# Kernel optimization log

Measured on AMD Instinct MI355X. Metric: run time of the kernel, lower is better.

The kernel has to match this reference:

```python
import jax, jax.numpy as jnp
import numpy as np

N_NODES = 50000
N_EDGES = 1600000
F_IN, F_LAT, F_EMB = 128, 256, 128
N_GRAPHS = 64


def _linear_init(key, out_dim, in_dim):
    scale = 1.0 / np.sqrt(in_dim)
    return jax.random.uniform(key, (out_dim, in_dim), jnp.float32, -scale, scale)


def setup_inputs() -> dict:
    key = jax.random.key(0)
    ks = jax.random.split(key, 12)
    x = jax.random.normal(ks[0], (N_NODES, F_IN), jnp.float32)
    edge_index = jax.random.randint(ks[1], (2, N_EDGES), 0, N_NODES, jnp.int64)
    batch = jnp.sort(jax.random.randint(ks[2], (N_NODES,), 0, N_GRAPHS, jnp.int64))
    return {
        'x': x,
        'edge_index': edge_index,
        'batch': batch,
        'W1l': _linear_init(ks[3], F_LAT, F_IN),
        'b1': jnp.zeros((F_LAT,), jnp.float32),
        'W1r': _linear_init(ks[4], F_LAT, F_IN),
        'W2l': _linear_init(ks[5], F_LAT, F_LAT),
        'b2': jnp.zeros((F_LAT,), jnp.float32),
        'W2r': _linear_init(ks[6], F_LAT, F_LAT),
        'W3l': _linear_init(ks[7], F_EMB, F_LAT),
        'b3': jnp.zeros((F_EMB,), jnp.float32),
        'W3r': _linear_init(ks[8], F_EMB, F_LAT),
    }


def _sage_conv(x, src, dst, deg_inv, Wl, bl, Wr):
    # mean aggregation of neighbor features: scatter-add then divide by in-degree
    agg = jax.ops.segment_sum(x[src], dst, num_segments=N_NODES) * deg_inv
    # PyG SAGEConv: lin_l(agg) + lin_r(x); lin_l has bias, lin_r does not
    return agg @ Wl.T + bl + x @ Wr.T


def reference(x, edge_index, batch, W1l, b1, W1r, W2l, b2, W2r, W3l, b3, W3r):
    src, dst = edge_index[0], edge_index[1]
    deg = jax.ops.segment_sum(jnp.ones((N_EDGES,), jnp.float32), dst, num_segments=N_NODES)
    deg_inv = jnp.where(deg > 0, 1.0 / deg, 0.0)[:, None]  # [N,1]
    h = jax.nn.relu(_sage_conv(x, src, dst, deg_inv, W1l, b1, W1r))
    h = jax.nn.relu(_sage_conv(h, src, dst, deg_inv, W2l, b2, W2r))
    h = jax.nn.relu(_sage_conv(h, src, dst, deg_inv, W3l, b3, W3r))
    # global_add_pool: per-graph sum over nodes
    return jax.ops.segment_sum(h, batch, num_segments=N_GRAPHS)
```

## Files before the change

kernel.cpp:

```cpp
#include <hip/hip_runtime.h>
#include <hip/hip_bf16.h>

#define N_NODES 50000
#define N_EDGES 1600000
#define N_GRAPHS 64

#define NBKT 250
#define BKT_NODES 200
#define BKT_CAP 7168
#define CHUNK 4096
#define NBB 391
#define NCVX 6250
#define NCVW 256
#define ZROW N_NODES

typedef short bf16x8 __attribute__((ext_vector_type(8)));
typedef float f32x4 __attribute__((ext_vector_type(4)));
typedef float f32x2 __attribute__((ext_vector_type(2)));

__device__ __forceinline__ float bf_lo(unsigned int u) { return __uint_as_float(u << 16); }
__device__ __forceinline__ float bf_hi(unsigned int u) { return __uint_as_float(u & 0xffff0000u); }
__device__ __forceinline__ unsigned short f2bf(float f) {
    unsigned int u = __float_as_uint(f);
    u = (u + 0x7fffu + ((u >> 16) & 1u)) >> 16;
    return (unsigned short)u;
}
__device__ __forceinline__ unsigned int pack2bf(float a, float b) {
    return (unsigned int)f2bf(a) | ((unsigned int)f2bf(b) << 16);
}
__device__ __forceinline__ unsigned int pack4fp8(float a, float b, float c, float d) {
    unsigned int q = __builtin_amdgcn_cvt_pk_fp8_f32(a, b, 0, false);
    q = __builtin_amdgcn_cvt_pk_fp8_f32(c, d, q, true);
    return q;
}
__device__ __forceinline__ void load_lds16(const void* g, void* l) {
    __builtin_amdgcn_global_load_lds(
        (const __attribute__((address_space(1))) void*)g,
        (__attribute__((address_space(3))) void*)l, 16, 0, 0);
}

__global__ __launch_bounds__(256) void k_front(
    const int* __restrict__ src, const int* __restrict__ dst,
    unsigned int* __restrict__ bucketed, int* __restrict__ gcnt,
    const float* __restrict__ x, unsigned short* __restrict__ A1x,
    unsigned char* __restrict__ x8,
    const float* __restrict__ W1l, const float* __restrict__ W1r,
    const float* __restrict__ W2l, const float* __restrict__ W2r,
    const float* __restrict__ W3l, const float* __restrict__ W3r,
    unsigned short* __restrict__ Wp1, unsigned short* __restrict__ Wp2,
    unsigned short* __restrict__ Wp3) {
    const int blk = blockIdx.x;
    const int t = threadIdx.x;

    if (blk < NBB) {
        __shared__ int lcnt[256];
        __shared__ int sc[256];
        __shared__ int lscan[256];
        __shared__ int gb[256];
        __shared__ unsigned int grouped[CHUNK];

        const int base = blk * CHUNK;
        const int ccnt = min(CHUNK, N_EDGES - base);
        lcnt[t] = 0;
        __syncthreads();

        unsigned int pk[CHUNK / 256];
        int rk[CHUNK / 256];
#pragma unroll
        for (int r = 0; r < CHUNK / 256; ++r) {
            int j = r * 256 + t;
            rk[r] = -1;
            if (j < ccnt) {
                int i = base + j;
                int s = src[i];
                int d = dst[i];
                int b = d / BKT_NODES;
                int dl = d - b * BKT_NODES;
                pk[r] = (unsigned int)s | ((unsigned int)dl << 16) | ((unsigned int)b << 24);
                rk[r] = atomicAdd(&lcnt[b], 1);
            }
        }
        __syncthreads();
        sc[t] = lcnt[t];
        __syncthreads();
        for (int off = 1; off < 256; off <<= 1) {
            int v = (t >= off) ? sc[t - off] : 0;
            __syncthreads();
            sc[t] += v;
            __syncthreads();
        }
        lscan[t] = sc[t] - lcnt[t];
        if (t < NBKT && lcnt[t] > 0) gb[t] = atomicAdd(&gcnt[t], lcnt[t]);
        __syncthreads();
#pragma unroll
        for (int r = 0; r < CHUNK / 256; ++r) {
            if (rk[r] >= 0) {
                int b = pk[r] >> 24;
                grouped[lscan[b] + rk[r]] = pk[r];
            }
        }
        __syncthreads();
#pragma unroll
        for (int r = 0; r < CHUNK / 256; ++r) {
            int j = r * 256 + t;
            if (j < ccnt) {
                unsigned int v = grouped[j];
                int b = v >> 24;
                int pos = gb[b] + (j - lscan[b]);
                if (pos < BKT_CAP) bucketed[b * BKT_CAP + pos] = v;
            }
        }
    } else if (blk < NBB + NCVX) {
        int i = (blk - NBB) * 256 + t;
        int r = i >> 5;
        int f4 = (i & 31) << 2;
        float4 v = *(const float4*)&x[(size_t)r * 128 + f4];
        uint2 o;
        o.x = pack2bf(v.x, v.y);
        o.y = pack2bf(v.z, v.w);
        *(uint2*)&A1x[(size_t)r * 256 + f4] = o;
        *(unsigned int*)&x8[(size_t)r * 128 + f4] = pack4fp8(v.x, v.y, v.z, v.w);
    } else {
        int i = (blk - NBB - NCVX) * 256 + t;
        const float* srcp;
        unsigned short* dstp;
        int sf4, dstride;
        if (i < 16384) {
            int h = i >> 13;
            i &= 8191;
            srcp = h ? W1r : W1l;
            dstp = Wp1 + (h ? 128 : 0);
            sf4 = 32; dstride = 256;
        } else if (i < 49152) {
            int j = i - 16384;
            int h = j >> 14;
            i = j & 16383;
            srcp = h ? W2r : W2l;
            dstp = Wp2 + (h ? 256 : 0);
            sf4 = 64; dstride = 512;
        } else {
            int j = i - 49152;
            int h = j >> 13;
            i = j & 8191;
            srcp = h ? W3r : W3l;
            dstp = Wp3 + (h ? 128 * 256 : 0);
            sf4 = 64; dstride = 256;
        }
        int r = i / sf4;
        int f4 = (i % sf4) * 4;
        float4 v = *(const float4*)&srcp[(size_t)r * (sf4 * 4) + f4];
        uint2 o;
        o.x = pack2bf(v.x, v.y);
        o.y = pack2bf(v.z, v.w);
        *(uint2*)&dstp[(size_t)r * dstride + f4] = o;
    }
}

__global__ __launch_bounds__(512) void k_place(const unsigned int* __restrict__ bucketed,
                                               const int* __restrict__ gcnt,
                                               int* __restrict__ offs,
                                               unsigned short* __restrict__ deg,
                                               unsigned short* __restrict__ ssrc) {
    __shared__ unsigned int ent[BKT_CAP];
    __shared__ unsigned short rks[BKT_CAP];
    __shared__ int lcnt[256];
    __shared__ int sc[256];
    __shared__ int lofs[256];
    __shared__ int gs;

    const int b = blockIdx.x;
    const int t = threadIdx.x;

    if (t < 256) sc[t] = (t < NBKT) ? (gcnt[t] + 3 * BKT_NODES) : 0;
    __syncthreads();
    for (int off = 1; off < 256; off <<= 1) {
        int u = 0;
        if (t < 256 && t >= off) u = sc[t - off];
        __syncthreads();
        if (t < 256) sc[t] += u;
        __syncthreads();
    }
    if (t == 0) gs = (b == 0) ? 0 : sc[b - 1];
    if (t < 256) lcnt[t] = 0;
    __syncthreads();

    const int cnt = min(gcnt[b], BKT_CAP);
    const unsigned int* eg = bucketed + (size_t)b * BKT_CAP;
    for (int i = t; i < cnt; i += 512) {
        unsigned int v = eg[i];
        ent[i] = v;
        int dl = (v >> 16) & 0xFF;
        rks[i] = (unsigned short)atomicAdd(&lcnt[dl], 1);
    }
    __syncthreads();
    int pc = 0;
    if (t < 256) {
        pc = (lcnt[t] + 3) & ~3;
        sc[t] = pc;
    }
    __syncthreads();
    for (int off = 1; off < 256; off <<= 1) {
        int u = 0;
        if (t < 256 && t >= off) u = sc[t - off];
        __syncthreads();
        if (t < 256) sc[t] += u;
        __syncthreads();
    }
    if (t < 256) lofs[t] = sc[t] - pc;
    __syncthreads();
    const int gstart = gs;
    if (t < BKT_NODES) {
        offs[b * BKT_NODES + t] = gstart + lofs[t];
        deg[b * BKT_NODES + t] = (unsigned short)lcnt[t];
    }
    for (int i = t; i < cnt; i += 512) {
        unsigned int v = ent[i];
        int dl = (v >> 16) & 0xFF;
        ssrc[gstart + lofs[dl] + (int)rks[i]] = (unsigned short)(v & 0xFFFF);
    }
    if (t < BKT_NODES) {
        int d = lcnt[t], pd = (d + 3) & ~3;
        int base = gstart + lofs[t];
        for (int j = d; j < pd; ++j) ssrc[base + j] = (unsigned short)ZROW;
    }
}

#define DEC_ADD(dw, base)                                             \
    {                                                                 \
        f32x2 lo_ = __builtin_amdgcn_cvt_pk_f32_fp8((dw), false);     \
        f32x2 hi_ = __builtin_amdgcn_cvt_pk_f32_fp8((dw), true);      \
        a[(base) + 0] += lo_.x;                                       \
        a[(base) + 1] += lo_.y;                                       \
        a[(base) + 2] += hi_.x;                                       \
        a[(base) + 3] += hi_.y;                                       \
    }

template <int F>
__global__ __launch_bounds__(256) void k_gather8(const unsigned char* __restrict__ in,
                                                 unsigned short* __restrict__ out,
                                                 int ostride,
                                                 const int* __restrict__ offs,
                                                 const unsigned short* __restrict__ deg,
                                                 const unsigned short* __restrict__ ssrc) {
    constexpr int TPN = F / 16;
    constexpr int NPB = 256 / TPN;
    int n = blockIdx.x * NPB + threadIdx.x / TPN;
    int f16 = (threadIdx.x % TPN) * 16;
    if (n >= N_NODES) return;
    int s0 = offs[n];
    int d = deg[n];
    int pd = (d + 3) & ~3;
    float a[16];
#pragma unroll
    for (int j = 0; j < 16; ++j) a[j] = 0.f;
    const unsigned char* inf = in + f16;
    for (int i = s0; i < s0 + pd; i += 4) {
        int e0 = ssrc[i], e1 = ssrc[i + 1], e2 = ssrc[i + 2], e3 = ssrc[i + 3];
        uint4 v0 = *(const uint4*)&inf[(size_t)e0 * F];
        uint4 v1 = *(const uint4*)&inf[(size_t)e1 * F];
        uint4 v2 = *(const uint4*)&inf[(size_t)e2 * F];
        uint4 v3 = *(const uint4*)&inf[(size_t)e3 * F];
        DEC_ADD(v0.x, 0) DEC_ADD(v0.y, 4) DEC_ADD(v0.z, 8) DEC_ADD(v0.w, 12)
        DEC_ADD(v1.x, 0) DEC_ADD(v1.y, 4) DEC_ADD(v1.z, 8) DEC_ADD(v1.w, 12)
        DEC_ADD(v2.x, 0) DEC_ADD(v2.y, 4) DEC_ADD(v2.z, 8) DEC_ADD(v2.w, 12)
        DEC_ADD(v3.x, 0) DEC_ADD(v3.y, 4) DEC_ADD(v3.z, 8) DEC_ADD(v3.w, 12)
    }
    float scl = (d > 0) ? 1.f / (float)d : 0.f;
    uint4 o0, o1;
    o0.x = pack2bf(a[0] * scl, a[1] * scl);
    o0.y = pack2bf(a[2] * scl, a[3] * scl);
    o0.z = pack2bf(a[4] * scl, a[5] * scl);
    o0.w = pack2bf(a[6] * scl, a[7] * scl);
    o1.x = pack2bf(a[8] * scl, a[9] * scl);
    o1.y = pack2bf(a[10] * scl, a[11] * scl);
    o1.z = pack2bf(a[12] * scl, a[13] * scl);
    o1.w = pack2bf(a[14] * scl, a[15] * scl);
    *(uint4*)&out[(size_t)n * ostride + f16] = o0;
    *(uint4*)&out[(size_t)n * ostride + f16 + 8] = o1;
}

template <int KSTEPS, bool RELU, bool BIAS, int FP8W>
__global__ __launch_bounds__(256) void k_gemm_mfma(const unsigned short* __restrict__ A,
                                                   const unsigned short* __restrict__ W,
                                                   const float* __restrict__ bias,
                                                   unsigned short* __restrict__ C,
                                                   int ldc, int coff,
                                                   unsigned char* __restrict__ fp8out,
                                                   int M) {
    constexpr int K = KSTEPS * 64;
    __shared__ unsigned short SH[32768];

    const int tid = threadIdx.x;
    const int lane = tid & 63;
    const int w = tid >> 6;
    const int row0 = blockIdx.x * 128;
    const int colb = blockIdx.y * 128;

    const int srow_b = w * 32 + (lane >> 3);
    const int slot = lane & 7;

    f32x4 acc[4][4];
#pragma unroll
    for (int i = 0; i < 4; ++i)
#pragma unroll
        for (int j = 0; j < 4; ++j) acc[i][j] = (f32x4){0.f, 0.f, 0.f, 0.f};

    const int m0 = (w >> 1) * 64;
    const int n0 = (w & 1) * 64;

    auto STAGE = [&](int b, int ks) {
        const int kk0 = ks * 64;
#pragma unroll
        for (int it = 0; it < 4; ++it) {
            int r = srow_b + it * 8;
            int sl = (slot ^ (r & 7)) << 3;
            int ra = min(row0 + r, M - 1);
            load_lds16(A + (size_t)ra * K + kk0 + sl,
                       (char*)SH + b * 16384 + w * 4096 + it * 1024);
            load_lds16(W + (size_t)(colb + r) * K + kk0 + sl,
                       (char*)SH + 32768 + b * 16384 + w * 4096 + it * 1024);
        }
    };

    STAGE(0, 0);
    __syncthreads();
    int cur = 0;

    for (int ks = 0; ks < KSTEPS; ++ks) {
        if (ks + 1 < KSTEPS) STAGE(cur ^ 1, ks + 1);

        const char* Ab = (const char*)SH + cur * 16384;
        const char* Wb = (const char*)SH + 32768 + cur * 16384;
        bf16x8 af[4][2], bfr[4][2];
#pragma unroll
        for (int mf = 0; mf < 4; ++mf)
#pragma unroll
            for (int kk = 0; kk < 2; ++kk) {
                int r = m0 + mf * 16 + (lane & 15);
                int sl = (kk * 4 + (lane >> 4)) ^ (r & 7);
                af[mf][kk] = *(const bf16x8*)(Ab + r * 128 + sl * 16);
            }
#pragma unroll
        for (int nf = 0; nf < 4; ++nf)
#pragma unroll
            for (int kk = 0; kk < 2; ++kk) {
                int r = n0 + nf * 16 + (lane & 15);
                int sl = (kk * 4 + (lane >> 4)) ^ (r & 7);
                bfr[nf][kk] = *(const bf16x8*)(Wb + r * 128 + sl * 16);
            }
#pragma unroll
        for (int mf = 0; mf < 4; ++mf)
#pragma unroll
            for (int nf = 0; nf < 4; ++nf)
#pragma unroll
                for (int kk = 0; kk < 2; ++kk)
                    acc[mf][nf] = __builtin_amdgcn_mfma_f32_16x16x32_bf16(
                        af[mf][kk], bfr[nf][kk], acc[mf][nf], 0, 0, 0);
        __syncthreads();
        cur ^= 1;
    }

    const bool do8 = (FP8W > 0) && (colb < FP8W);

#pragma unroll
    for (int mf = 0; mf < 4; ++mf) {
#pragma unroll
        for (int nf = 0; nf < 4; ++nf) {
            int cl = n0 + nf * 16 + (lane & 15);
            int c = colb + cl;
            float bv = 0.f;
            if constexpr (BIAS) bv = bias[c];
#pragma unroll
            for (int r = 0; r < 4; ++r) {
                int ml = m0 + mf * 16 + ((lane >> 4) << 2) + r;
                int m = row0 + ml;
                if (m < M) {
                    float v = acc[mf][nf][r] + bv;
                    if constexpr (RELU) v = fmaxf(v, 0.f);
                    unsigned short bf = f2bf(v);
                    C[(size_t)m * ldc + coff + c] = bf;
                    if constexpr (FP8W > 0)
                        if (do8) SH[ml * 136 + cl] = bf;
                }
            }
        }
    }

    if constexpr (FP8W > 0) {
        if (do8) {
            __syncthreads();
#pragma unroll
            for (int q0 = 0; q0 < 1024; q0 += 256) {
                int q = q0 + tid;
                int row = q >> 3;
                int m = row0 + row;
                if (m < M) {
                    int cg = (q & 7) << 4;
                    const unsigned short* tp = SH + row * 136 + cg;
                    uint4 w0 = *(const uint4*)tp;
                    uint4 w1 = *(const uint4*)(tp + 8);
                    uint4 o;
                    o.x = pack4fp8(bf_lo(w0.x), bf_hi(w0.x), bf_lo(w0.y), bf_hi(w0.y));
                    o.y = pack4fp8(bf_lo(w0.z), bf_hi(w0.z), bf_lo(w0.w), bf_hi(w0.w));
                    o.z = pack4fp8(bf_lo(w1.x), bf_hi(w1.x), bf_lo(w1.y), bf_hi(w1.y));
                    o.w = pack4fp8(bf_lo(w1.z), bf_hi(w1.z), bf_lo(w1.w), bf_hi(w1.w));
                    *(uint4*)&fp8out[(size_t)m * FP8W + colb + cg] = o;
                }
            }
        }
    }
}

__global__ __launch_bounds__(256) void k_final8(const unsigned char* __restrict__ t3l8,
                                                const unsigned short* __restrict__ t3,
                                                const float* __restrict__ b3,
                                                const int* __restrict__ offs,
                                                const unsigned short* __restrict__ deg,
                                                const unsigned short* __restrict__ ssrc,
                                                const int* __restrict__ batch,
                                                float* __restrict__ out) {
    __shared__ float sm[16][128];
    __shared__ int bsh[16];
    const int t = threadIdx.x;
    const int sub = t >> 4;
    const int f8 = (t & 15) * 8;
    const int n = blockIdx.x * 16 + sub;

    int s0 = offs[n];
    int d = deg[n];
    int pd = (d + 3) & ~3;
    float a[8];
#pragma unroll
    for (int j = 0; j < 8; ++j) a[j] = 0.f;
    const unsigned char* inf = t3l8 + f8;
    for (int i = s0; i < s0 + pd; i += 4) {
        int e0 = ssrc[i], e1 = ssrc[i + 1], e2 = ssrc[i + 2], e3 = ssrc[i + 3];
        uint2 v0 = *(const uint2*)&inf[(size_t)e0 * 128];
        uint2 v1 = *(const uint2*)&inf[(size_t)e1 * 128];
        uint2 v2 = *(const uint2*)&inf[(size_t)e2 * 128];
        uint2 v3 = *(const uint2*)&inf[(size_t)e3 * 128];
        DEC_ADD(v0.x, 0) DEC_ADD(v0.y, 4)
        DEC_ADD(v1.x, 0) DEC_ADD(v1.y, 4)
        DEC_ADD(v2.x, 0) DEC_ADD(v2.y, 4)
        DEC_ADD(v3.x, 0) DEC_ADD(v3.y, 4)
    }
    float scl = (d > 0) ? 1.f / (float)d : 0.f;
    float4 bv0 = *(const float4*)&b3[f8];
    float4 bv1 = *(const float4*)&b3[f8 + 4];
    uint4 tr = *(const uint4*)&t3[(size_t)n * 256 + 128 + f8];
    float tv[8] = {bf_lo(tr.x), bf_hi(tr.x), bf_lo(tr.y), bf_hi(tr.y),
                   bf_lo(tr.z), bf_hi(tr.z), bf_lo(tr.w), bf_hi(tr.w)};
    float bb[8] = {bv0.x, bv0.y, bv0.z, bv0.w, bv1.x, bv1.y, bv1.z, bv1.w};
#pragma unroll
    for (int j = 0; j < 8; ++j)
        sm[sub][f8 + j] = fmaxf(a[j] * scl + bb[j] + tv[j], 0.f);
    if ((t & 15) == 0) bsh[sub] = batch[n];
    __syncthreads();

    if (t < 128) {
        float local = 0.f;
        int cur = -1;
#pragma unroll
        for (int k = 0; k < 16; ++k) {
            int b = bsh[k];
            if (b != cur) {
                if (cur >= 0) atomicAdd(&out[(size_t)cur * 128 + t], local);
                local = 0.f;
                cur = b;
            }
            local += sm[k][t];
        }
        if (cur >= 0) atomicAdd(&out[(size_t)cur * 128 + t], local);
    }
}

extern "C" void kernel_launch(void* const* d_in, const int* in_sizes, int n_in,
                              void* d_out, int out_size, void* d_ws, size_t ws_size,
                              hipStream_t stream) {
    const float* x   = (const float*)d_in[0];
    const int* ei    = (const int*)d_in[1];
    const int* batch = (const int*)d_in[2];
    const float* W1l = (const float*)d_in[3];
    const float* b1  = (const float*)d_in[4];
    const float* W1r = (const float*)d_in[5];
    const float* W2l = (const float*)d_in[6];
    const float* b2  = (const float*)d_in[7];
    const float* W2r = (const float*)d_in[8];
    const float* W3l = (const float*)d_in[9];
    const float* b3  = (const float*)d_in[10];
    const float* W3r = (const float*)d_in[11];
    const int* src = ei;
    const int* dst = ei + N_EDGES;
    float* out = (float*)d_out;

    size_t off = 0;
    auto carve = [&](size_t bytes) {
        void* p = (char*)d_ws + off;
        off += (bytes + 255) & ~(size_t)255;
        return p;
    };
    int* gcnt   = (int*)carve(256 * 4);
    int* offs   = (int*)carve((size_t)N_NODES * 4);
    unsigned short* deg  = (unsigned short*)carve((size_t)N_NODES * 2);
    unsigned short* ssrc = (unsigned short*)carve((size_t)(N_EDGES + NBKT * 3 * BKT_NODES) * 2);
    unsigned short* A1   = (unsigned short*)carve((size_t)N_NODES * 256 * 2);
    unsigned short* A2   = (unsigned short*)carve((size_t)N_NODES * 512 * 2);
    unsigned short* A3   = (unsigned short*)carve((size_t)N_NODES * 256 * 2);
    void* t3region = carve((size_t)N_NODES * 256 * 2);
    unsigned int* bucketed = (unsigned int*)t3region;
    unsigned short* t3 = (unsigned short*)t3region;
    unsigned char* x8   = (unsigned char*)carve((size_t)(N_NODES + 1) * 128);
    unsigned char* h18  = (unsigned char*)carve((size_t)(N_NODES + 1) * 256);
    unsigned char* t3l8 = (unsigned char*)carve((size_t)(N_NODES + 1) * 128);
    unsigned short* Wp1 = (unsigned short*)carve((size_t)256 * 256 * 2);
    unsigned short* Wp2 = (unsigned short*)carve((size_t)256 * 512 * 2);
    unsigned short* Wp3 = (unsigned short*)carve((size_t)256 * 256 * 2);

    hipMemsetAsync(gcnt, 0, 256 * 4, stream);
    hipMemsetAsync(d_out, 0, (size_t)out_size * 4, stream);
    hipMemsetAsync(x8 + (size_t)ZROW * 128, 0, 128, stream);
    hipMemsetAsync(h18 + (size_t)ZROW * 256, 0, 256, stream);
    hipMemsetAsync(t3l8 + (size_t)ZROW * 128, 0, 128, stream);

    k_front<<<NBB + NCVX + NCVW, 256, 0, stream>>>(src, dst, bucketed, gcnt,
                                                   x, A1 + 128, x8,
                                                   W1l, W1r, W2l, W2r, W3l, W3r,
                                                   Wp1, Wp2, Wp3);
    k_place<<<NBKT, 512, 0, stream>>>(bucketed, gcnt, offs, deg, ssrc);

    const dim3 ggrid((N_NODES + 127) / 128, 2);

    k_gather8<128><<<(N_NODES + 31) / 32, 256, 0, stream>>>(x8, A1, 256, offs, deg, ssrc);
    k_gemm_mfma<4, true, true, 256><<<ggrid, 256, 0, stream>>>(A1, Wp1, b1, A2, 512, 256, h18, N_NODES);

    k_gather8<256><<<(N_NODES + 15) / 16, 256, 0, stream>>>(h18, A2, 512, offs, deg, ssrc);
    k_gemm_mfma<8, true, true, 0><<<ggrid, 256, 0, stream>>>(A2, Wp2, b2, A3, 256, 0, nullptr, N_NODES);

    k_gemm_mfma<4, false, false, 128><<<ggrid, 256, 0, stream>>>(A3, Wp3, nullptr, t3, 256, 0, t3l8, N_NODES);
    k_final8<<<N_NODES / 16, 256, 0, stream>>>(t3l8, t3, b3, offs, deg, ssrc, batch, out);
}
```

Before: 319.8 us.

## Software-pipeline gather loops, vectorize index loads, fold zero-row memsets into front kernel

The gather kernels now prefetch the next group of four neighbor rows before accumulating the current group. They load four source indices with a single ushort4 read, which needs bucket offsets aligned to four. To keep that alignment, k_place rounds each bucket count up to a multiple of four, and the ssrc allocation grows to match. Three small memset launches for the zero padding rows are replaced by writes inside k_front. Together these aim to hide gather latency and cut launch overhead, at the cost of more live registers.

Measured after the change: 314.1 us. About the same (-1.8%).

```diff
diff --git a/kernel.cpp b/kernel.cpp
--- a/kernel.cpp
+++ b/kernel.cpp
@@ -43,7 +43,8 @@
     const int* __restrict__ src, const int* __restrict__ dst,
     unsigned int* __restrict__ bucketed, int* __restrict__ gcnt,
     const float* __restrict__ x, unsigned short* __restrict__ A1x,
-    unsigned char* __restrict__ x8,
+    unsigned char* __restrict__ x8, unsigned char* __restrict__ h18,
+    unsigned char* __restrict__ t3l8,
     const float* __restrict__ W1l, const float* __restrict__ W1r,
     const float* __restrict__ W2l, const float* __restrict__ W2r,
     const float* __restrict__ W3l, const float* __restrict__ W3r,
@@ -120,6 +121,12 @@
         o.y = pack2bf(v.z, v.w);
         *(uint2*)&A1x[(size_t)r * 256 + f4] = o;
         *(unsigned int*)&x8[(size_t)r * 128 + f4] = pack4fp8(v.x, v.y, v.z, v.w);
+        if (blk == NBB && t < 32) {
+            uint4 z = make_uint4(0, 0, 0, 0);
+            if (t < 8) *(uint4*)&x8[(size_t)ZROW * 128 + t * 16] = z;
+            else if (t < 24) *(uint4*)&h18[(size_t)ZROW * 256 + (t - 8) * 16] = z;
+            else *(uint4*)&t3l8[(size_t)ZROW * 128 + (t - 24) * 16] = z;
+        }
     } else {
         int i = (blk - NBB - NCVX) * 256 + t;
         const float* srcp;
@@ -171,7 +178,7 @@
     const int b = blockIdx.x;
     const int t = threadIdx.x;
 
-    if (t < 256) sc[t] = (t < NBKT) ? (gcnt[t] + 3 * BKT_NODES) : 0;
+    if (t < 256) sc[t] = (t < NBKT) ? (((gcnt[t] + 3) & ~3) + 3 * BKT_NODES) : 0;
     __syncthreads();
     for (int off = 1; off < 256; off <<= 1) {
         int u = 0;
@@ -234,6 +241,7 @@
         a[(base) + 2] += hi_.x;                                       \
         a[(base) + 3] += hi_.y;                                       \
     }
+#define DEC_ADD4(v) { DEC_ADD((v).x, 0) DEC_ADD((v).y, 4) DEC_ADD((v).z, 8) DEC_ADD((v).w, 12) }
 
 template <int F>
 __global__ __launch_bounds__(256) void k_gather8(const unsigned char* __restrict__ in,
@@ -254,16 +262,22 @@
 #pragma unroll
     for (int j = 0; j < 16; ++j) a[j] = 0.f;
     const unsigned char* inf = in + f16;
-    for (int i = s0; i < s0 + pd; i += 4) {
-        int e0 = ssrc[i], e1 = ssrc[i + 1], e2 = ssrc[i + 2], e3 = ssrc[i + 3];
-        uint4 v0 = *(const uint4*)&inf[(size_t)e0 * F];
-        uint4 v1 = *(const uint4*)&inf[(size_t)e1 * F];
-        uint4 v2 = *(const uint4*)&inf[(size_t)e2 * F];
-        uint4 v3 = *(const uint4*)&inf[(size_t)e3 * F];
-        DEC_ADD(v0.x, 0) DEC_ADD(v0.y, 4) DEC_ADD(v0.z, 8) DEC_ADD(v0.w, 12)
-        DEC_ADD(v1.x, 0) DEC_ADD(v1.y, 4) DEC_ADD(v1.z, 8) DEC_ADD(v1.w, 12)
-        DEC_ADD(v2.x, 0) DEC_ADD(v2.y, 4) DEC_ADD(v2.z, 8) DEC_ADD(v2.w, 12)
-        DEC_ADD(v3.x, 0) DEC_ADD(v3.y, 4) DEC_ADD(v3.z, 8) DEC_ADD(v3.w, 12)
+    if (pd > 0) {
+        ushort4 es = *(const ushort4*)&ssrc[s0];
+        uint4 c0 = *(const uint4*)&inf[(size_t)es.x * F];
+        uint4 c1 = *(const uint4*)&inf[(size_t)es.y * F];
+        uint4 c2 = *(const uint4*)&inf[(size_t)es.z * F];
+        uint4 c3 = *(const uint4*)&inf[(size_t)es.w * F];
+        for (int i = s0 + 4; i < s0 + pd; i += 4) {
+            ushort4 ns = *(const ushort4*)&ssrc[i];
+            uint4 n0 = *(const uint4*)&inf[(size_t)ns.x * F];
+            uint4 n1 = *(const uint4*)&inf[(size_t)ns.y * F];
+            uint4 n2 = *(const uint4*)&inf[(size_t)ns.z * F];
+            uint4 n3 = *(const uint4*)&inf[(size_t)ns.w * F];
+            DEC_ADD4(c0) DEC_ADD4(c1) DEC_ADD4(c2) DEC_ADD4(c3)
+            c0 = n0; c1 = n1; c2 = n2; c3 = n3;
+        }
+        DEC_ADD4(c0) DEC_ADD4(c1) DEC_ADD4(c2) DEC_ADD4(c3)
     }
     float scl = (d > 0) ? 1.f / (float)d : 0.f;
     uint4 o0, o1;
@@ -433,16 +447,28 @@
 #pragma unroll
     for (int j = 0; j < 8; ++j) a[j] = 0.f;
     const unsigned char* inf = t3l8 + f8;
-    for (int i = s0; i < s0 + pd; i += 4) {
-        int e0 = ssrc[i], e1 = ssrc[i + 1], e2 = ssrc[i + 2], e3 = ssrc[i + 3];
-        uint2 v0 = *(const uint2*)&inf[(size_t)e0 * 128];
-        uint2 v1 = *(const uint2*)&inf[(size_t)e1 * 128];
-        uint2 v2 = *(const uint2*)&inf[(size_t)e2 * 128];
-        uint2 v3 = *(const uint2*)&inf[(size_t)e3 * 128];
-        DEC_ADD(v0.x, 0) DEC_ADD(v0.y, 4)
-        DEC_ADD(v1.x, 0) DEC_ADD(v1.y, 4)
-        DEC_ADD(v2.x, 0) DEC_ADD(v2.y, 4)
-        DEC_ADD(v3.x, 0) DEC_ADD(v3.y, 4)
+    if (pd > 0) {
+        ushort4 es = *(const ushort4*)&ssrc[s0];
+        uint2 c0 = *(const uint2*)&inf[(size_t)es.x * 128];
+        uint2 c1 = *(const uint2*)&inf[(size_t)es.y * 128];
+        uint2 c2 = *(const uint2*)&inf[(size_t)es.z * 128];
+        uint2 c3 = *(const uint2*)&inf[(size_t)es.w * 128];
+        for (int i = s0 + 4; i < s0 + pd; i += 4) {
+            ushort4 ns = *(const ushort4*)&ssrc[i];
+            uint2 n0 = *(const uint2*)&inf[(size_t)ns.x * 128];
+            uint2 n1 = *(const uint2*)&inf[(size_t)ns.y * 128];
+            uint2 n2 = *(const uint2*)&inf[(size_t)ns.z * 128];
+            uint2 n3 = *(const uint2*)&inf[(size_t)ns.w * 128];
+            DEC_ADD(c0.x, 0) DEC_ADD(c0.y, 4)
+            DEC_ADD(c1.x, 0) DEC_ADD(c1.y, 4)
+            DEC_ADD(c2.x, 0) DEC_ADD(c2.y, 4)
+            DEC_ADD(c3.x, 0) DEC_ADD(c3.y, 4)
+            c0 = n0; c1 = n1; c2 = n2; c3 = n3;
+        }
+        DEC_ADD(c0.x, 0) DEC_ADD(c0.y, 4)
+        DEC_ADD(c1.x, 0) DEC_ADD(c1.y, 4)
+        DEC_ADD(c2.x, 0) DEC_ADD(c2.y, 4)
+        DEC_ADD(c3.x, 0) DEC_ADD(c3.y, 4)
     }
     float scl = (d > 0) ? 1.f / (float)d : 0.f;
     float4 bv0 = *(const float4*)&b3[f8];
@@ -502,7 +528,7 @@
     int* gcnt   = (int*)carve(256 * 4);
     int* offs   = (int*)carve((size_t)N_NODES * 4);
     unsigned short* deg  = (unsigned short*)carve((size_t)N_NODES * 2);
-    unsigned short* ssrc = (unsigned short*)carve((size_t)(N_EDGES + NBKT * 3 * BKT_NODES) * 2);
+    unsigned short* ssrc = (unsigned short*)carve((size_t)(N_EDGES + NBKT * 1024) * 2);
     unsigned short* A1   = (unsigned short*)carve((size_t)N_NODES * 256 * 2);
     unsigned short* A2   = (unsigned short*)carve((size_t)N_NODES * 512 * 2);
     unsigned short* A3   = (unsigned short*)carve((size_t)N_NODES * 256 * 2);
@@ -518,12 +544,9 @@
 
     hipMemsetAsync(gcnt, 0, 256 * 4, stream);
     hipMemsetAsync(d_out, 0, (size_t)out_size * 4, stream);
-    hipMemsetAsync(x8 + (size_t)ZROW * 128, 0, 128, stream);
-    hipMemsetAsync(h18 + (size_t)ZROW * 256, 0, 256, stream);
-    hipMemsetAsync(t3l8 + (size_t)ZROW * 128, 0, 128, stream);
 
     k_front<<<NBB + NCVX + NCVW, 256, 0, stream>>>(src, dst, bucketed, gcnt,
-                                                   x, A1 + 128, x8,
+                                                   x, A1 + 128, x8, h18, t3l8,
                                                    W1l, W1r, W2l, W2r, W3l, W3r,
                                                    Wp1, Wp2, Wp3);
     k_place<<<NBKT, 512, 0, stream>>>(bucketed, gcnt, offs, deg, ssrc);
```
